# Optimization experiments

Hardware: AMD Instinct MI355X
Metric: run time of the kernel (lower is better)

## Reference

```python
import jax, jax.numpy as jnp
import numpy as np

B, N, D = 4, 2048, 1024
H, HD = 16, 64          # heads, head dim
ROT = 64                # rotary dims (full head)
SCALE = HD ** -0.5


def _rotate_half(x):
    # interleaved pair rotation: (c r) with r=2 -> (-x2, x1)
    x = x.reshape(x.shape[:-1] + (-1, 2))
    x1, x2 = x[..., 0], x[..., 1]
    return jnp.stack((-x2, x1), axis=-1).reshape(x.shape[:-2] + (-1,))


def _rope(t, pos_enc):
    # t: [b,h,n,c], pos_enc: [1,n,rot] -> broadcast over heads
    pe = pos_enc[:, None, : t.shape[-2], :]          # [1,1,n,rot]
    t_rot, t_pass = t[..., :ROT], t[..., ROT:]
    t_rot = t_rot * jnp.cos(pe) + _rotate_half(t_rot) * jnp.sin(pe)
    return jnp.concatenate((t_rot, t_pass), axis=-1)


def setup_inputs() -> dict:
    key = jax.random.key(0)
    ks = jax.random.split(key, 16)
    s = 0.02
    return {
        "query": jax.random.normal(ks[0], (B, N, D), jnp.float32),
        "key": jax.random.normal(ks[1], (B, N, D), jnp.float32),
        "value": jax.random.normal(ks[2], (B, N, D), jnp.float32),
        "pad_mask": jax.random.randint(ks[3], (B, N), 0, 2) > 0,
        "pos_enc": jax.random.uniform(ks[4], (1, N, ROT), jnp.float32),
        "Wq": jax.random.normal(ks[5], (D, D), jnp.float32) * s,
        "bq": jnp.zeros((D,), jnp.float32),
        "Wk": jax.random.normal(ks[6], (D, D), jnp.float32) * s,
        "bk": jnp.zeros((D,), jnp.float32),
        "Wv": jax.random.normal(ks[7], (D, D), jnp.float32) * s,
        "bv": jnp.zeros((D,), jnp.float32),
        "Wo": jax.random.normal(ks[8], (D, D), jnp.float32) * s,
        "bo": jnp.zeros((D,), jnp.float32),
    }


def reference(query, key, value, pad_mask, pos_enc, Wq, bq, Wk, bk, Wv, bv, Wo, bo):
    def split_heads(x):
        return x.reshape(x.shape[0], x.shape[1], H, HD).transpose(0, 2, 1, 3)  # b h n c

    q = split_heads(query @ Wq + bq) * SCALE
    k = split_heads(key @ Wk + bk)
    v = split_heads(value @ Wv + bv)

    q = _rope(q, pos_enc)
    k = _rope(k, pos_enc)

    attn = jnp.einsum("bhic,bhjc->bhij", q, k)
    neg = -jnp.finfo(attn.dtype).max
    attn = jnp.where(pad_mask[:, None, None, :], neg, attn)
    attn = jax.nn.softmax(attn, axis=-1)

    o = jnp.einsum("bhij,bhjc->bhic", attn, v)
    o = o.transpose(0, 2, 1, 3).reshape(o.shape[0], o.shape[2], H * HD)  # b n (h c)
    return o @ Wo + bo
```

## Files before the change

kernel.cpp:

```cpp
#include <hip/hip_runtime.h>

#define B_ 4
#define N_ 2048
#define D_ 1024
#define H_ 16
#define HD_ 64
#define QSCALE_ 0.18033688011112042f

typedef __bf16 bf16x8 __attribute__((ext_vector_type(8)));
typedef float f32x4 __attribute__((ext_vector_type(4)));

#if __has_builtin(__builtin_amdgcn_exp2f)
#define EXP2(x) __builtin_amdgcn_exp2f(x)
#else
#define EXP2(x) exp2f(x)
#endif

__device__ __forceinline__ f32x4 mfma16(bf16x8 a, bf16x8 b, f32x4 c) {
    return __builtin_amdgcn_mfma_f32_16x16x32_bf16(a, b, c, 0, 0, 0);
}

__device__ __forceinline__ void gload16(const void* g, void* l) {
    __builtin_amdgcn_global_load_lds(
        (const __attribute__((address_space(1))) void*)g,
        (__attribute__((address_space(3))) void*)l, 16, 0, 0);
}

__device__ __forceinline__ unsigned pack2(float x, float y) {
    __bf16 a = (__bf16)x, b = (__bf16)y;
    unsigned ua = __builtin_bit_cast(unsigned short, a);
    unsigned ub = __builtin_bit_cast(unsigned short, b);
    return ua | (ub << 16);
}

__global__ __launch_bounds__(256) void pre_kernel(
    const float* __restrict__ q, const float* __restrict__ k, const float* __restrict__ v,
    __bf16* __restrict__ xb,
    const float* __restrict__ W0, const float* __restrict__ W1,
    const float* __restrict__ W2, const float* __restrict__ W3,
    __bf16* __restrict__ T0, __bf16* __restrict__ T1,
    __bf16* __restrict__ T2, __bf16* __restrict__ T3,
    const float* __restrict__ pe, const int* __restrict__ mask,
    unsigned* __restrict__ cstab, float* __restrict__ maskf)
{
    const int y = blockIdx.y;
    const int x = blockIdx.x;
    const int t = threadIdx.x;

    if (y < 3) {
        const float* src = (y == 0) ? q : (y == 1) ? k : v;
        __bf16* dst = xb + (size_t)y * 8388608;
        size_t i = ((size_t)x * 256 + t) * 8;
        float4 a = *(const float4*)(src + i);
        float4 b = *(const float4*)(src + i + 4);
        bf16x8 o;
        o[0] = (__bf16)a.x; o[1] = (__bf16)a.y; o[2] = (__bf16)a.z; o[3] = (__bf16)a.w;
        o[4] = (__bf16)b.x; o[5] = (__bf16)b.y; o[6] = (__bf16)b.z; o[7] = (__bf16)b.w;
        *(bf16x8*)(dst + i) = o;
        return;
    }
    if (x < 1024) {
        const int which = x >> 8;
        const float* W = (which == 0) ? W0 : (which == 1) ? W1 : (which == 2) ? W2 : W3;
        __bf16* Wt = (which == 0) ? T0 : (which == 1) ? T1 : (which == 2) ? T2 : T3;
        const int k0 = ((x >> 4) & 15) * 64, n0 = (x & 15) * 64;
        __shared__ float T[64][65];
#pragma unroll
        for (int i = 0; i < 4; ++i) {
            int row = i * 16 + (t >> 4);
            int c4 = (t & 15) * 4;
            float4 vv = *(const float4*)(W + (size_t)(k0 + row) * D_ + n0 + c4);
            T[row][c4] = vv.x; T[row][c4 + 1] = vv.y; T[row][c4 + 2] = vv.z; T[row][c4 + 3] = vv.w;
        }
        __syncthreads();
#pragma unroll
        for (int i = 0; i < 2; ++i) {
            int task = i * 256 + t;
            int nrow = task >> 3, ks = task & 7;
            bf16x8 o;
#pragma unroll
            for (int e = 0; e < 8; ++e) o[e] = (__bf16)T[ks * 8 + e][nrow];
            *(bf16x8*)(Wt + (size_t)(n0 + nrow) * D_ + k0 + ks * 8) = o;
        }
        return;
    }
    if (x < 1568) {
        int i = (x - 1024) * 256 + t;
        if (i < N_ * HD_) {
            float vv = pe[i];
            __bf16 cb = (__bf16)cosf(vv), sb = (__bf16)sinf(vv);
            unsigned cu = __builtin_bit_cast(unsigned short, cb);
            unsigned su = __builtin_bit_cast(unsigned short, sb);
            cstab[i] = cu | (su << 16);
        }
        if (i < B_ * N_) maskf[i] = mask[i] ? -1e30f : 0.0f;
    }
}

__global__ void prep_kernel(const float* __restrict__ pe, const int* __restrict__ mask,
                            unsigned* __restrict__ cstab, float* __restrict__ maskf) {
    int i = blockIdx.x * 256 + threadIdx.x;
    if (i < N_ * HD_) {
        float v = pe[i];
        __bf16 cb = (__bf16)cosf(v), sb = (__bf16)sinf(v);
        unsigned cu = __builtin_bit_cast(unsigned short, cb);
        unsigned su = __builtin_bit_cast(unsigned short, sb);
        cstab[i] = cu | (su << 16);
    }
    if (i < B_ * N_) maskf[i] = mask[i] ? -1e30f : 0.0f;
}

__global__ __launch_bounds__(256) void tw_kernel(const float* __restrict__ W, __bf16* __restrict__ Wt) {
    __shared__ float T[64][65];
    const int k0 = blockIdx.x * 64, n0 = blockIdx.y * 64;
    const int t = threadIdx.x;
#pragma unroll
    for (int i = 0; i < 4; ++i) {
        int row = i * 16 + (t >> 4);
        int c4 = (t & 15) * 4;
        float4 v = *(const float4*)(W + (size_t)(k0 + row) * D_ + n0 + c4);
        T[row][c4] = v.x; T[row][c4 + 1] = v.y; T[row][c4 + 2] = v.z; T[row][c4 + 3] = v.w;
    }
    __syncthreads();
#pragma unroll
    for (int i = 0; i < 2; ++i) {
        int task = i * 256 + t;
        int nrow = task >> 3, ks = task & 7;
        bf16x8 o;
#pragma unroll
        for (int e = 0; e < 8; ++e) o[e] = (__bf16)T[ks * 8 + e][nrow];
        *(bf16x8*)(Wt + (size_t)(n0 + nrow) * D_ + k0 + ks * 8) = o;
    }
}

__global__ __launch_bounds__(256) void tw3_kernel(
    const float* __restrict__ W0, const float* __restrict__ W1, const float* __restrict__ W2,
    __bf16* __restrict__ T0, __bf16* __restrict__ T1, __bf16* __restrict__ T2)
{
    const float* W = (blockIdx.z == 0) ? W0 : (blockIdx.z == 1) ? W1 : W2;
    __bf16* Wt = (blockIdx.z == 0) ? T0 : (blockIdx.z == 1) ? T1 : T2;
    __shared__ float T[64][65];
    const int k0 = blockIdx.x * 64, n0 = blockIdx.y * 64;
    const int t = threadIdx.x;
#pragma unroll
    for (int i = 0; i < 4; ++i) {
        int row = i * 16 + (t >> 4);
        int c4 = (t & 15) * 4;
        float4 v = *(const float4*)(W + (size_t)(k0 + row) * D_ + n0 + c4);
        T[row][c4] = v.x; T[row][c4 + 1] = v.y; T[row][c4 + 2] = v.z; T[row][c4 + 3] = v.w;
    }
    __syncthreads();
#pragma unroll
    for (int i = 0; i < 2; ++i) {
        int task = i * 256 + t;
        int nrow = task >> 3, ks = task & 7;
        bf16x8 o;
#pragma unroll
        for (int e = 0; e < 8; ++e) o[e] = (__bf16)T[ks * 8 + e][nrow];
        *(bf16x8*)(Wt + (size_t)(n0 + nrow) * D_ + k0 + ks * 8) = o;
    }
}

__global__ __launch_bounds__(256) void proj_v6(
    const __bf16* __restrict__ Xb,
    const __bf16* __restrict__ WtQ, const __bf16* __restrict__ WtK, const __bf16* __restrict__ WtV,
    const float* __restrict__ bQ, const float* __restrict__ bK, const float* __restrict__ bV,
    const unsigned* __restrict__ cstab,
    __bf16* __restrict__ dq, __bf16* __restrict__ dk, __bf16* __restrict__ dv)
{
    __shared__ __align__(16) char smem[35072];
    __bf16* As = (__bf16*)smem;
    __bf16* Bs = (__bf16*)(smem + 16384);

    const int which = blockIdx.y >> 3;
    const __bf16* X   = Xb + (size_t)which * 8388608;
    const __bf16* Wt  = (which == 0) ? WtQ : (which == 1) ? WtK : WtV;
    const float* bias = (which == 0) ? bQ  : (which == 1) ? bK  : bV;
    __bf16* dst       = (which == 0) ? dq  : (which == 1) ? dk  : dv;
    const int mode = which;

    const int tid = threadIdx.x;
    const int lane = tid & 63, w = tid >> 6;
    const int wr = w >> 1, wc = w & 1;
    const int r16 = lane & 15, g = lane >> 4;
    const int m0 = blockIdx.x * 128;
    const int n0 = (blockIdx.y & 7) * 128;
    const int srow8 = tid >> 3, slot = tid & 7;

    f32x4 acc[4][4];
#pragma unroll
    for (int m = 0; m < 4; ++m)
#pragma unroll
        for (int n = 0; n < 4; ++n) acc[m][n] = (f32x4){0.f, 0.f, 0.f, 0.f};

    for (int kt = 0; kt < 16; ++kt) {
#pragma unroll
        for (int j = 0; j < 4; ++j) {
            int row = j * 32 + srow8;
            const char* srcA = (const char*)X + ((size_t)(m0 + row) * D_ + kt * 64) * 2
                               + ((slot ^ (row & 7)) << 4);
            gload16(srcA, (char*)As + j * 4096 + w * 1024);
            const char* srcB = (const char*)Wt + ((size_t)(n0 + row) * D_ + kt * 64) * 2
                               + ((slot ^ (row & 7)) << 4);
            gload16(srcB, (char*)Bs + j * 4096 + w * 1024);
        }
        __syncthreads();
#pragma unroll
        for (int kk = 0; kk < 2; ++kk) {
            bf16x8 aF[4], bF[4];
#pragma unroll
            for (int m = 0; m < 4; ++m) {
                int row = wr * 64 + m * 16 + r16;
                aF[m] = *(const bf16x8*)((char*)As + row * 128 + (((kk * 4 + g) ^ (row & 7)) << 4));
            }
#pragma unroll
            for (int n = 0; n < 4; ++n) {
                int row = wc * 64 + n * 16 + r16;
                bF[n] = *(const bf16x8*)((char*)Bs + row * 128 + (((kk * 4 + g) ^ (row & 7)) << 4));
            }
#pragma unroll
            for (int m = 0; m < 4; ++m)
#pragma unroll
                for (int n = 0; n < 4; ++n)
                    acc[m][n] = mfma16(aF[m], bF[n], acc[m][n]);
        }
        __syncthreads();
    }

    if (mode <= 1) {
#pragma unroll
        for (int m = 0; m < 4; ++m)
#pragma unroll
            for (int n = 0; n < 4; ++n) {
                int col = n0 + wc * 64 + n * 16 + r16;
                int h = col >> 6, hd = col & 63;
#pragma unroll
                for (int j = 0; j < 4; ++j) {
                    int bn = m0 + wr * 64 + m * 16 + g * 4 + j;
                    int np = bn & (N_ - 1), b = bn >> 11;
                    float val = acc[m][n][j] + bias[col];
                    if (mode == 0) val *= QSCALE_;
                    float other = __shfl_xor(val, 1);
                    unsigned cs = cstab[np * HD_ + hd];
                    float c = __uint_as_float(cs << 16);
                    float sn = __uint_as_float(cs & 0xffff0000u);
                    val = val * c + ((col & 1) ? other : -other) * sn;
                    dst[((size_t)(b * H_ + h) * N_ + np) * HD_ + hd] = (__bf16)val;
                }
            }
    } else {
        __bf16* T = (__bf16*)smem;
        __syncthreads();
#pragma unroll
        for (int m = 0; m < 4; ++m)
#pragma unroll
            for (int n = 0; n < 4; ++n) {
                int c = wc * 64 + n * 16 + r16;
                float bs = bias[n0 + c];
#pragma unroll
                for (int j = 0; j < 4; ++j) {
                    int sr = wr * 64 + m * 16 + g * 4 + j;
                    T[c * 136 + sr] = (__bf16)(acc[m][n][j] + bs);
                }
            }
        __syncthreads();
        const int b = m0 >> 11, np0 = m0 & (N_ - 1);
#pragma unroll
        for (int i = 0; i < 8; ++i) {
            int task = i * 256 + tid;
            int trow = task >> 4, ch = task & 15;
            int colg = n0 + trow;
            int h = colg >> 6, hd = colg & 63;
            bf16x8 vv = *(const bf16x8*)&T[trow * 136 + ch * 8];
            *(bf16x8*)(dst + (((size_t)(b * H_ + h) * HD_ + hd) * N_ + np0 + ch * 8)) = vv;
        }
    }
}

__global__ __launch_bounds__(256) void proj_v5(
    const float* __restrict__ Xq, const float* __restrict__ Xk, const float* __restrict__ Xv,
    const __bf16* __restrict__ WtQ, const __bf16* __restrict__ WtK, const __bf16* __restrict__ WtV,
    const float* __restrict__ bQ, const float* __restrict__ bK, const float* __restrict__ bV,
    const unsigned* __restrict__ cstab,
    __bf16* __restrict__ dq, __bf16* __restrict__ dk, __bf16* __restrict__ dv)
{
    __shared__ __align__(16) char smem[35072];
    __bf16* As = (__bf16*)smem;
    __bf16* Bs = (__bf16*)(smem + 16384);

    const int which = blockIdx.y >> 3;
    const float* X    = (which == 0) ? Xq  : (which == 1) ? Xk  : Xv;
    const __bf16* Wt  = (which == 0) ? WtQ : (which == 1) ? WtK : WtV;
    const float* bias = (which == 0) ? bQ  : (which == 1) ? bK  : bV;
    __bf16* dst       = (which == 0) ? dq  : (which == 1) ? dk  : dv;
    const int mode = which;

    const int tid = threadIdx.x;
    const int lane = tid & 63, w = tid >> 6;
    const int wr = w >> 1, wc = w & 1;
    const int r16 = lane & 15, g = lane >> 4;
    const int m0 = blockIdx.x * 128;
    const int n0 = (blockIdx.y & 7) * 128;
    const int srow8 = tid >> 3, slot = tid & 7;

    f32x4 acc[4][4];
#pragma unroll
    for (int m = 0; m < 4; ++m)
#pragma unroll
        for (int n = 0; n < 4; ++n) acc[m][n] = (f32x4){0.f, 0.f, 0.f, 0.f};

    for (int kt = 0; kt < 16; ++kt) {
        float4 va0[4], va1[4];
#pragma unroll
        for (int i = 0; i < 4; ++i) {
            int row = i * 32 + srow8;
            const float* s = X + (size_t)(m0 + row) * D_ + kt * 64 + slot * 8;
            va0[i] = *(const float4*)s;
            va1[i] = *(const float4*)(s + 4);
        }
#pragma unroll
        for (int j = 0; j < 4; ++j) {
            int row = j * 32 + srow8;
            const char* src = (const char*)Wt + ((size_t)(n0 + row) * D_ + kt * 64) * 2
                              + ((slot ^ (row & 7)) << 4);
            gload16(src, (char*)Bs + j * 4096 + w * 1024);
        }
#pragma unroll
        for (int i = 0; i < 4; ++i) {
            int row = i * 32 + srow8;
            bf16x8 bv;
            bv[0] = (__bf16)va0[i].x; bv[1] = (__bf16)va0[i].y;
            bv[2] = (__bf16)va0[i].z; bv[3] = (__bf16)va0[i].w;
            bv[4] = (__bf16)va1[i].x; bv[5] = (__bf16)va1[i].y;
            bv[6] = (__bf16)va1[i].z; bv[7] = (__bf16)va1[i].w;
            *(bf16x8*)((char*)As + row * 128 + ((slot ^ (row & 7)) << 4)) = bv;
        }
        __syncthreads();
#pragma unroll
        for (int kk = 0; kk < 2; ++kk) {
            bf16x8 aF[4], bF[4];
#pragma unroll
            for (int m = 0; m < 4; ++m) {
                int row = wr * 64 + m * 16 + r16;
                aF[m] = *(const bf16x8*)((char*)As + row * 128 + (((kk * 4 + g) ^ (row & 7)) << 4));
            }
#pragma unroll
            for (int n = 0; n < 4; ++n) {
                int row = wc * 64 + n * 16 + r16;
                bF[n] = *(const bf16x8*)((char*)Bs + row * 128 + (((kk * 4 + g) ^ (row & 7)) << 4));
            }
#pragma unroll
            for (int m = 0; m < 4; ++m)
#pragma unroll
                for (int n = 0; n < 4; ++n)
                    acc[m][n] = mfma16(aF[m], bF[n], acc[m][n]);
        }
        __syncthreads();
    }

    if (mode <= 1) {
#pragma unroll
        for (int m = 0; m < 4; ++m)
#pragma unroll
            for (int n = 0; n < 4; ++n) {
                int col = n0 + wc * 64 + n * 16 + r16;
                int h = col >> 6, hd = col & 63;
#pragma unroll
                for (int j = 0; j < 4; ++j) {
                    int bn = m0 + wr * 64 + m * 16 + g * 4 + j;
                    int np = bn & (N_ - 1), b = bn >> 11;
                    float val = acc[m][n][j] + bias[col];
                    if (mode == 0) val *= QSCALE_;
                    float other = __shfl_xor(val, 1);
                    unsigned cs = cstab[np * HD_ + hd];
                    float c = __uint_as_float(cs << 16);
                    float sn = __uint_as_float(cs & 0xffff0000u);
                    val = val * c + ((col & 1) ? other : -other) * sn;
                    dst[((size_t)(b * H_ + h) * N_ + np) * HD_ + hd] = (__bf16)val;
                }
            }
    } else {
        __bf16* T = (__bf16*)smem;
        __syncthreads();
#pragma unroll
        for (int m = 0; m < 4; ++m)
#pragma unroll
            for (int n = 0; n < 4; ++n) {
                int c = wc * 64 + n * 16 + r16;
                float bs = bias[n0 + c];
#pragma unroll
                for (int j = 0; j < 4; ++j) {
                    int sr = wr * 64 + m * 16 + g * 4 + j;
                    T[c * 136 + sr] = (__bf16)(acc[m][n][j] + bs);
                }
            }
        __syncthreads();
        const int b = m0 >> 11, np0 = m0 & (N_ - 1);
#pragma unroll
        for (int i = 0; i < 8; ++i) {
            int task = i * 256 + tid;
            int trow = task >> 4, ch = task & 15;
            int colg = n0 + trow;
            int h = colg >> 6, hd = colg & 63;
            bf16x8 vv = *(const bf16x8*)&T[trow * 136 + ch * 8];
            *(bf16x8*)(dst + (((size_t)(b * H_ + h) * HD_ + hd) * N_ + np0 + ch * 8)) = vv;
        }
    }
}

__global__ __launch_bounds__(512, 4) void attn_v8(
    const __bf16* __restrict__ qws, const __bf16* __restrict__ kws,
    const __bf16* __restrict__ vtws, const float* __restrict__ maskf,
    __bf16* __restrict__ ows)
{
    __shared__ __align__(16) __bf16 Ks0[4096], Ks1[4096];
    __shared__ __align__(16) __bf16 Vs0[4096], Vs1[4096];
    __shared__ __align__(16) char Pbuf[16384];

    const int tid = threadIdx.x;
    const int lane = tid & 63, w = tid >> 6;
    const int r16 = lane & 15, g = lane >> 4;

    const int lid = blockIdx.x;
    const int virt = (lid & 7) * 64 + (lid >> 3);
    const int bh = virt >> 3;
    const int b = bh >> 4, h = bh & 15;
    const int q0 = (virt & 7) * 256;
    const int srow8 = tid >> 3, slot = tid & 7;

    bf16x8 qF[2][2];
#pragma unroll
    for (int qq = 0; qq < 2; ++qq) {
        const __bf16* qb = qws + ((size_t)bh * N_ + q0 + w * 32 + qq * 16 + r16) * HD_ + g * 8;
        qF[qq][0] = *(const bf16x8*)qb;
        qF[qq][1] = *(const bf16x8*)(qb + 32);
    }

    bf16x8 onesF;
#pragma unroll
    for (int e = 0; e < 8; ++e) onesF[e] = (__bf16)1.0f;

    const char* kbase = (const char*)(kws + (size_t)bh * N_ * HD_);
    const char* vbase = (const char*)(vtws + (size_t)bh * HD_ * N_);
    const float* mbase = maskf + b * N_;
    char* Pw = Pbuf + w * 2048;

    f32x4 o[2][4];
    f32x4 lacc[2];
#pragma unroll
    for (int qq = 0; qq < 2; ++qq) {
        lacc[qq] = (f32x4){0.f, 0.f, 0.f, 0.f};
#pragma unroll
        for (int n = 0; n < 4; ++n) o[qq][n] = (f32x4){0.f, 0.f, 0.f, 0.f};
    }

#define STAGE_(KD, VD, kt) {                                                          \
    gload16(kbase + (size_t)((kt) * 64 + srow8) * 128 + ((slot ^ (srow8 & 7)) << 4),  \
            (char*)(KD) + w * 1024);                                                  \
    gload16(vbase + (size_t)srow8 * (N_ * 2) + (kt) * 128 + ((slot ^ (srow8 & 7)) << 4), \
            (char*)(VD) + w * 1024);                                                  \
    }

#define TILE_(KB, VB, KN, VN, kt) {                                                   \
    if ((kt) + 1 < 32) STAGE_(KN, VN, (kt) + 1);                                      \
    f32x4 s0[4], s1[4];                                                               \
    _Pragma("unroll")                                                                 \
    for (int n = 0; n < 4; ++n) {                                                     \
        f32x4 mb = *(const f32x4*)(mbase + (kt) * 64 + n * 16 + g * 4);               \
        s0[n] = mb; s1[n] = mb;                                                       \
    }                                                                                 \
    __builtin_amdgcn_s_setprio(1);                                                    \
    _Pragma("unroll")                                                                 \
    for (int n = 0; n < 4; ++n) {                                                     \
        int row = n * 16 + r16;                                                       \
        bf16x8 kF0 = *(const bf16x8*)((const char*)(KB) + row * 128 + ((g ^ (row & 7)) << 4));        \
        bf16x8 kF1 = *(const bf16x8*)((const char*)(KB) + row * 128 + (((4 + g) ^ (row & 7)) << 4));  \
        s0[n] = mfma16(kF0, qF[0][0], s0[n]);                                         \
        s0[n] = mfma16(kF1, qF[0][1], s0[n]);                                         \
        s1[n] = mfma16(kF0, qF[1][0], s1[n]);                                         \
        s1[n] = mfma16(kF1, qF[1][1], s1[n]);                                         \
    }                                                                                 \
    __builtin_amdgcn_s_setprio(0);                                                    \
    bf16x8 pF0[2], pF1[2];                                                            \
    _Pragma("unroll")                                                                 \
    for (int n = 0; n < 4; ++n) {                                                     \
        int u0 = ((n * 2 + (g >> 1)) ^ (r16 & 7));                                    \
        int off = (g & 1) * 2;                                                        \
        *(unsigned*)(Pw + r16 * 128 + u0 * 16 + off * 4)       = pack2(EXP2(s0[n][0]), EXP2(s0[n][1])); \
        *(unsigned*)(Pw + r16 * 128 + u0 * 16 + (off + 1) * 4) = pack2(EXP2(s0[n][2]), EXP2(s0[n][3])); \
    }                                                                                 \
    _Pragma("unroll")                                                                 \
    for (int kk = 0; kk < 2; ++kk)                                                    \
        pF0[kk] = *(const bf16x8*)(Pw + r16 * 128 + (((kk * 4 + g) ^ (r16 & 7)) << 4)); \
    lacc[0] = mfma16(onesF, pF0[0], lacc[0]);                                         \
    lacc[0] = mfma16(onesF, pF0[1], lacc[0]);                                         \
    _Pragma("unroll")                                                                 \
    for (int n = 0; n < 4; ++n) {                                                     \
        int u0 = ((n * 2 + (g >> 1)) ^ (r16 & 7));                                    \
        int off = (g & 1) * 2;                                                        \
        *(unsigned*)(Pw + r16 * 128 + u0 * 16 + off * 4)       = pack2(EXP2(s1[n][0]), EXP2(s1[n][1])); \
        *(unsigned*)(Pw + r16 * 128 + u0 * 16 + (off + 1) * 4) = pack2(EXP2(s1[n][2]), EXP2(s1[n][3])); \
    }                                                                                 \
    _Pragma("unroll")                                                                 \
    for (int kk = 0; kk < 2; ++kk)                                                    \
        pF1[kk] = *(const bf16x8*)(Pw + r16 * 128 + (((kk * 4 + g) ^ (r16 & 7)) << 4)); \
    lacc[1] = mfma16(onesF, pF1[0], lacc[1]);                                         \
    lacc[1] = mfma16(onesF, pF1[1], lacc[1]);                                         \
    __builtin_amdgcn_s_setprio(1);                                                    \
    _Pragma("unroll")                                                                 \
    for (int n = 0; n < 4; ++n) {                                                     \
        int row = n * 16 + r16;                                                       \
        bf16x8 vF0 = *(const bf16x8*)((const char*)(VB) + row * 128 + ((g ^ (row & 7)) << 4));        \
        bf16x8 vF1 = *(const bf16x8*)((const char*)(VB) + row * 128 + (((4 + g) ^ (row & 7)) << 4));  \
        o[0][n] = mfma16(vF0, pF0[0], o[0][n]);                                       \
        o[0][n] = mfma16(vF1, pF0[1], o[0][n]);                                       \
        o[1][n] = mfma16(vF0, pF1[0], o[1][n]);                                       \
        o[1][n] = mfma16(vF1, pF1[1], o[1][n]);                                       \
    }                                                                                 \
    __builtin_amdgcn_s_setprio(0);                                                    \
    __syncthreads(); }

    STAGE_(Ks0, Vs0, 0);
    __syncthreads();

    for (int kt = 0; kt < 32; kt += 2) {
        TILE_(Ks0, Vs0, Ks1, Vs1, kt);
        TILE_(Ks1, Vs1, Ks0, Vs0, kt + 1);
    }
#undef TILE_
#undef STAGE_

#pragma unroll
    for (int qq = 0; qq < 2; ++qq) {
        float inv = 1.0f / lacc[qq][0];
#pragma unroll
        for (int n = 0; n < 4; ++n) {
            int u0 = ((n * 2 + (g >> 1)) ^ (r16 & 7));
            int off = (g & 1) * 2;
            *(unsigned*)(Pw + r16 * 128 + u0 * 16 + off * 4)       = pack2(o[qq][n][0] * inv, o[qq][n][1] * inv);
            *(unsigned*)(Pw + r16 * 128 + u0 * 16 + (off + 1) * 4) = pack2(o[qq][n][2] * inv, o[qq][n][3] * inv);
        }
        int qrow = q0 + w * 32 + qq * 16 + r16;
#pragma unroll
        for (int kk = 0; kk < 2; ++kk) {
            bf16x8 v = *(const bf16x8*)(Pw + r16 * 128 + (((kk * 4 + g) ^ (r16 & 7)) << 4));
            *(bf16x8*)(ows + ((size_t)(b * N_ + qrow)) * D_ + h * HD_ + kk * 32 + g * 8) = v;
        }
    }
}

__global__ __launch_bounds__(256) void gemm_out_v2(
    const __bf16* __restrict__ A, const __bf16* __restrict__ Wt,
    const float* __restrict__ bias, float* __restrict__ out)
{
    __shared__ __align__(16) __bf16 As[8192], Bs[8192];

    const int tid = threadIdx.x;
    const int lane = tid & 63, w = tid >> 6;
    const int wr = w >> 1, wc = w & 1;
    const int r16 = lane & 15, g = lane >> 4;
    const int m0 = blockIdx.x * 128;
    const int n0 = blockIdx.y * 128;
    const int srow8 = tid >> 3, slot = tid & 7;

    f32x4 acc[4][4];
#pragma unroll
    for (int m = 0; m < 4; ++m)
#pragma unroll
        for (int n = 0; n < 4; ++n) acc[m][n] = (f32x4){0.f, 0.f, 0.f, 0.f};

    for (int kt = 0; kt < 16; ++kt) {
#pragma unroll
        for (int j = 0; j < 4; ++j) {
            int row = j * 32 + srow8;
            const char* srcA = (const char*)A + ((size_t)(m0 + row) * D_ + kt * 64) * 2
                               + ((slot ^ (row & 7)) << 4);
            gload16(srcA, (char*)As + j * 4096 + w * 1024);
            const char* srcB = (const char*)Wt + ((size_t)(n0 + row) * D_ + kt * 64) * 2
                               + ((slot ^ (row & 7)) << 4);
            gload16(srcB, (char*)Bs + j * 4096 + w * 1024);
        }
        __syncthreads();
#pragma unroll
        for (int kk = 0; kk < 2; ++kk) {
            bf16x8 aF[4], bF[4];
#pragma unroll
            for (int m = 0; m < 4; ++m) {
                int row = wr * 64 + m * 16 + r16;
                aF[m] = *(const bf16x8*)((char*)As + row * 128 + (((kk * 4 + g) ^ (row & 7)) << 4));
            }
#pragma unroll
            for (int n = 0; n < 4; ++n) {
                int row = wc * 64 + n * 16 + r16;
                bF[n] = *(const bf16x8*)((char*)Bs + row * 128 + (((kk * 4 + g) ^ (row & 7)) << 4));
            }
#pragma unroll
            for (int m = 0; m < 4; ++m)
#pragma unroll
                for (int n = 0; n < 4; ++n)
                    acc[m][n] = mfma16(aF[m], bF[n], acc[m][n]);
        }
        __syncthreads();
    }

#pragma unroll
    for (int m = 0; m < 4; ++m)
#pragma unroll
        for (int n = 0; n < 4; ++n) {
            int col = n0 + wc * 64 + n * 16 + r16;
            float bs = bias[col];
#pragma unroll
            for (int j = 0; j < 4; ++j) {
                int bn = m0 + wr * 64 + m * 16 + g * 4 + j;
                out[(size_t)bn * D_ + col] = acc[m][n][j] + bs;
            }
        }
}

extern "C" void kernel_launch(void* const* d_in, const int* in_sizes, int n_in,
                              void* d_out, int out_size, void* d_ws, size_t ws_size,
                              hipStream_t stream)
{
    const float* query = (const float*)d_in[0];
    const float* key   = (const float*)d_in[1];
    const float* value = (const float*)d_in[2];
    const int* mask    = (const int*)d_in[3];
    const float* pos_enc = (const float*)d_in[4];
    const float* Wq = (const float*)d_in[5];
    const float* bq = (const float*)d_in[6];
    const float* Wk = (const float*)d_in[7];
    const float* bk = (const float*)d_in[8];
    const float* Wv = (const float*)d_in[9];
    const float* bv = (const float*)d_in[10];
    const float* Wo = (const float*)d_in[11];
    const float* bo = (const float*)d_in[12];
    float* out = (float*)d_out;

    char* ws = (char*)d_ws;
    const size_t MB16 = (size_t)16 * 1024 * 1024;
    const size_t MB2  = (size_t)2 * 1024 * 1024;
    const size_t need_big = 3 * MB16 + 4 * MB16 + 4 * MB2 + 524288 + 32768;
    const size_t need_small = 4 * MB16 + 524288 + 32768;

    if (ws_size >= need_big) {
        __bf16* Xb    = (__bf16*)(ws);
        __bf16* qws   = (__bf16*)(ws + 3 * MB16);
        __bf16* kws   = (__bf16*)(ws + 4 * MB16);
        __bf16* vtws  = (__bf16*)(ws + 5 * MB16);
        __bf16* ows   = (__bf16*)(ws + 6 * MB16);
        __bf16* wtQ   = (__bf16*)(ws + 7 * MB16);
        __bf16* wtK   = (__bf16*)(ws + 7 * MB16 + MB2);
        __bf16* wtV   = (__bf16*)(ws + 7 * MB16 + 2 * MB2);
        __bf16* wtO   = (__bf16*)(ws + 7 * MB16 + 3 * MB2);
        unsigned* cstab = (unsigned*)(ws + 7 * MB16 + 4 * MB2);
        float* maskf  = (float*)(ws + 7 * MB16 + 4 * MB2 + 524288);

        hipLaunchKernelGGL(pre_kernel, dim3(4096, 4), dim3(256), 0, stream,
                           query, key, value, Xb, Wq, Wk, Wv, Wo, wtQ, wtK, wtV, wtO,
                           pos_enc, mask, cstab, maskf);
        hipLaunchKernelGGL(proj_v6, dim3(64, 24), dim3(256), 0, stream,
                           Xb, wtQ, wtK, wtV, bq, bk, bv, cstab, qws, kws, vtws);
        hipLaunchKernelGGL(attn_v8, dim3(512), dim3(512), 0, stream,
                           qws, kws, vtws, maskf, ows);
        hipLaunchKernelGGL(gemm_out_v2, dim3(64, 8), dim3(256), 0, stream, ows, wtO, bo, out);
    } else {
        if (ws_size < need_small) return;
        __bf16* qws   = (__bf16*)(ws);
        __bf16* kws   = (__bf16*)(ws + MB16);
        __bf16* vtws  = (__bf16*)(ws + 2 * MB16);
        __bf16* ows   = (__bf16*)(ws + 3 * MB16);
        unsigned* cstab = (unsigned*)(ws + 4 * MB16);
        float* maskf  = (float*)(ws + 4 * MB16 + 524288);
        __bf16* wtQ   = (__bf16*)(ws + 3 * MB16);
        __bf16* wtK   = wtQ + (size_t)D_ * D_;
        __bf16* wtV   = wtK + (size_t)D_ * D_;
        __bf16* wtO   = (__bf16*)(ws);

        hipLaunchKernelGGL(prep_kernel, dim3(512), dim3(256), 0, stream, pos_enc, mask, cstab, maskf);
        hipLaunchKernelGGL(tw3_kernel, dim3(16, 16, 3), dim3(256), 0, stream, Wq, Wk, Wv, wtQ, wtK, wtV);
        hipLaunchKernelGGL(proj_v5, dim3(64, 24), dim3(256), 0, stream,
                           query, key, value, wtQ, wtK, wtV, bq, bk, bv, cstab, qws, kws, vtws);
        hipLaunchKernelGGL(attn_v8, dim3(512), dim3(512), 0, stream,
                           qws, kws, vtws, maskf, ows);
        hipLaunchKernelGGL(tw_kernel, dim3(16, 16), dim3(256), 0, stream, Wo, wtO);
        hipLaunchKernelGGL(gemm_out_v2, dim3(64, 8), dim3(256), 0, stream, ows, wtO, bo, out);
    }
}
```

Measured before the change: 206.4 us.

## Halve attention query tile per block and double grid size

Measured after the change: 227.2 us. 1.1x slower.

```diff
diff --git a/kernel.cpp b/kernel.cpp
--- a/kernel.cpp
+++ b/kernel.cpp
@@ -408,7 +408,7 @@
     }
 }
 
-__global__ __launch_bounds__(512, 4) void attn_v8(
+__global__ __launch_bounds__(512, 4) void attn_v9(
     const __bf16* __restrict__ qws, const __bf16* __restrict__ kws,
     const __bf16* __restrict__ vtws, const float* __restrict__ maskf,
     __bf16* __restrict__ ows)
@@ -422,18 +422,17 @@
     const int r16 = lane & 15, g = lane >> 4;
 
     const int lid = blockIdx.x;
-    const int virt = (lid & 7) * 64 + (lid >> 3);
-    const int bh = virt >> 3;
+    const int virt = (lid & 7) * 128 + (lid >> 3);
+    const int bh = virt >> 4;
     const int b = bh >> 4, h = bh & 15;
-    const int q0 = (virt & 7) * 256;
+    const int q0 = (virt & 15) * 128;
     const int srow8 = tid >> 3, slot = tid & 7;
 
-    bf16x8 qF[2][2];
-#pragma unroll
-    for (int qq = 0; qq < 2; ++qq) {
-        const __bf16* qb = qws + ((size_t)bh * N_ + q0 + w * 32 + qq * 16 + r16) * HD_ + g * 8;
-        qF[qq][0] = *(const bf16x8*)qb;
-        qF[qq][1] = *(const bf16x8*)(qb + 32);
+    bf16x8 qF0, qF1;
+    {
+        const __bf16* qb = qws + ((size_t)bh * N_ + q0 + w * 16 + r16) * HD_ + g * 8;
+        qF0 = *(const bf16x8*)qb;
+        qF1 = *(const bf16x8*)(qb + 32);
     }
 
     bf16x8 onesF;
@@ -445,14 +444,10 @@
     const float* mbase = maskf + b * N_;
     char* Pw = Pbuf + w * 2048;
 
-    f32x4 o[2][4];
-    f32x4 lacc[2];
-#pragma unroll
-    for (int qq = 0; qq < 2; ++qq) {
-        lacc[qq] = (f32x4){0.f, 0.f, 0.f, 0.f};
-#pragma unroll
-        for (int n = 0; n < 4; ++n) o[qq][n] = (f32x4){0.f, 0.f, 0.f, 0.f};
-    }
+    f32x4 o[4];
+    f32x4 lacc = (f32x4){0.f, 0.f, 0.f, 0.f};
+#pragma unroll
+    for (int n = 0; n < 4; ++n) o[n] = (f32x4){0.f, 0.f, 0.f, 0.f};
 
 #define STAGE_(KD, VD, kt) {                                                          \
     gload16(kbase + (size_t)((kt) * 64 + srow8) * 128 + ((slot ^ (srow8 & 7)) << 4),  \
@@ -463,59 +458,42 @@
 
 #define TILE_(KB, VB, KN, VN, kt) {                                                   \
     if ((kt) + 1 < 32) STAGE_(KN, VN, (kt) + 1);                                      \
-    f32x4 s0[4], s1[4];                                                               \
+    f32x4 s[4];                                                                       \
     _Pragma("unroll")                                                                 \
-    for (int n = 0; n < 4; ++n) {                                                     \
-        f32x4 mb = *(const f32x4*)(mbase + (kt) * 64 + n * 16 + g * 4);               \
-        s0[n] = mb; s1[n] = mb;                                                       \
-    }                                                                                 \
+    for (int n = 0; n < 4; ++n)                                                       \
+        s[n] = *(const f32x4*)(mbase + (kt) * 64 + n * 16 + g * 4);                   \
     __builtin_amdgcn_s_setprio(1);                                                    \
     _Pragma("unroll")                                                                 \
     for (int n = 0; n < 4; ++n) {                                                     \
         int row = n * 16 + r16;                                                       \
         bf16x8 kF0 = *(const bf16x8*)((const char*)(KB) + row * 128 + ((g ^ (row & 7)) << 4));        \
         bf16x8 kF1 = *(const bf16x8*)((const char*)(KB) + row * 128 + (((4 + g) ^ (row & 7)) << 4));  \
-        s0[n] = mfma16(kF0, qF[0][0], s0[n]);                                         \
-        s0[n] = mfma16(kF1, qF[0][1], s0[n]);                                         \
-        s1[n] = mfma16(kF0, qF[1][0], s1[n]);                                         \
-        s1[n] = mfma16(kF1, qF[1][1], s1[n]);                                         \
+        s[n] = mfma16(kF0, qF0, s[n]);                                                \
+        s[n] = mfma16(kF1, qF1, s[n]);                                                \
     }                                                                                 \
     __builtin_amdgcn_s_setprio(0);                                                    \
-    bf16x8 pF0[2], pF1[2];                                                            \
+    bf16x8 pF[2];                                                                     \
     _Pragma("unroll")                                                                 \
     for (int n = 0; n < 4; ++n) {                                                     \
         int u0 = ((n * 2 + (g >> 1)) ^ (r16 & 7));                                    \
-        int off = (g & 1) * 2;                                                        \
-        *(unsigned*)(Pw + r16 * 128 + u0 * 16 + off * 4)       = pack2(EXP2(s0[n][0]), EXP2(s0[n][1])); \
-        *(unsigned*)(Pw + r16 * 128 + u0 * 16 + (off + 1) * 4) = pack2(EXP2(s0[n][2]), EXP2(s0[n][3])); \
+        unsigned lo = pack2(EXP2(s[n][0]), EXP2(s[n][1]));                            \
+        unsigned hi = pack2(EXP2(s[n][2]), EXP2(s[n][3]));                            \
+        *(unsigned long long*)(Pw + r16 * 128 + u0 * 16 + (g & 1) * 8) =              \
+            ((unsigned long long)hi << 32) | lo;                                      \
     }                                                                                 \
     _Pragma("unroll")                                                                 \
     for (int kk = 0; kk < 2; ++kk)                                                    \
-        pF0[kk] = *(const bf16x8*)(Pw + r16 * 128 + (((kk * 4 + g) ^ (r16 & 7)) << 4)); \
-    lacc[0] = mfma16(onesF, pF0[0], lacc[0]);                                         \
-    lacc[0] = mfma16(onesF, pF0[1], lacc[0]);                                         \
-    _Pragma("unroll")                                                                 \
-    for (int n = 0; n < 4; ++n) {                                                     \
-        int u0 = ((n * 2 + (g >> 1)) ^ (r16 & 7));                                    \
-        int off = (g & 1) * 2;                                                        \
-        *(unsigned*)(Pw + r16 * 128 + u0 * 16 + off * 4)       = pack2(EXP2(s1[n][0]), EXP2(s1[n][1])); \
-        *(unsigned*)(Pw + r16 * 128 + u0 * 16 + (off + 1) * 4) = pack2(EXP2(s1[n][2]), EXP2(s1[n][3])); \
-    }                                                                                 \
-    _Pragma("unroll")                                                                 \
-    for (int kk = 0; kk < 2; ++kk)                                                    \
-        pF1[kk] = *(const bf16x8*)(Pw + r16 * 128 + (((kk * 4 + g) ^ (r16 & 7)) << 4)); \
-    lacc[1] = mfma16(onesF, pF1[0], lacc[1]);                                         \
-    lacc[1] = mfma16(onesF, pF1[1], lacc[1]);                                         \
+        pF[kk] = *(const bf16x8*)(Pw + r16 * 128 + (((kk * 4 + g) ^ (r16 & 7)) << 4)); \
+    lacc = mfma16(onesF, pF[0], lacc);                                                \
+    lacc = mfma16(onesF, pF[1], lacc);                                                \
     __builtin_amdgcn_s_setprio(1);                                                    \
     _Pragma("unroll")                                                                 \
     for (int n = 0; n < 4; ++n) {                                                     \
         int row = n * 16 + r16;                                                       \
         bf16x8 vF0 = *(const bf16x8*)((const char*)(VB) + row * 128 + ((g ^ (row & 7)) << 4));        \
         bf16x8 vF1 = *(const bf16x8*)((const char*)(VB) + row * 128 + (((4 + g) ^ (row & 7)) << 4));  \
-        o[0][n] = mfma16(vF0, pF0[0], o[0][n]);                                       \
-        o[0][n] = mfma16(vF1, pF0[1], o[0][n]);                                       \
-        o[1][n] = mfma16(vF0, pF1[0], o[1][n]);                                       \
-        o[1][n] = mfma16(vF1, pF1[1], o[1][n]);                                       \
+        o[n] = mfma16(vF0, pF[0], o[n]);                                              \
+        o[n] = mfma16(vF1, pF[1], o[n]);                                              \
     }                                                                                 \
     __builtin_amdgcn_s_setprio(0);                                                    \
     __syncthreads(); }
@@ -530,17 +508,17 @@
 #undef TILE_
 #undef STAGE_
 
-#pragma unroll
-    for (int qq = 0; qq < 2; ++qq) {
-        float inv = 1.0f / lacc[qq][0];
+    {
+        float inv = 1.0f / lacc[0];
 #pragma unroll
         for (int n = 0; n < 4; ++n) {
             int u0 = ((n * 2 + (g >> 1)) ^ (r16 & 7));
-            int off = (g & 1) * 2;
-            *(unsigned*)(Pw + r16 * 128 + u0 * 16 + off * 4)       = pack2(o[qq][n][0] * inv, o[qq][n][1] * inv);
-            *(unsigned*)(Pw + r16 * 128 + u0 * 16 + (off + 1) * 4) = pack2(o[qq][n][2] * inv, o[qq][n][3] * inv);
-        }
-        int qrow = q0 + w * 32 + qq * 16 + r16;
+            unsigned lo = pack2(o[n][0] * inv, o[n][1] * inv);
+            unsigned hi = pack2(o[n][2] * inv, o[n][3] * inv);
+            *(unsigned long long*)(Pw + r16 * 128 + u0 * 16 + (g & 1) * 8) =
+                ((unsigned long long)hi << 32) | lo;
+        }
+        int qrow = q0 + w * 16 + r16;
 #pragma unroll
         for (int kk = 0; kk < 2; ++kk) {
             bf16x8 v = *(const bf16x8*)(Pw + r16 * 128 + (((kk * 4 + g) ^ (r16 & 7)) << 4));
@@ -660,7 +638,7 @@
                            pos_enc, mask, cstab, maskf);
         hipLaunchKernelGGL(proj_v6, dim3(64, 24), dim3(256), 0, stream,
                            Xb, wtQ, wtK, wtV, bq, bk, bv, cstab, qws, kws, vtws);
-        hipLaunchKernelGGL(attn_v8, dim3(512), dim3(512), 0, stream,
+        hipLaunchKernelGGL(attn_v9, dim3(1024), dim3(512), 0, stream,
                            qws, kws, vtws, maskf, ows);
         hipLaunchKernelGGL(gemm_out_v2, dim3(64, 8), dim3(256), 0, stream, ows, wtO, bo, out);
     } else {
@@ -680,7 +658,7 @@
         hipLaunchKernelGGL(tw3_kernel, dim3(16, 16, 3), dim3(256), 0, stream, Wq, Wk, Wv, wtQ, wtK, wtV);
         hipLaunchKernelGGL(proj_v5, dim3(64, 24), dim3(256), 0, stream,
                            query, key, value, wtQ, wtK, wtV, bq, bk, bv, cstab, qws, kws, vtws);
-        hipLaunchKernelGGL(attn_v8, dim3(512), dim3(512), 0, stream,
+        hipLaunchKernelGGL(attn_v9, dim3(1024), dim3(512), 0, stream,
                            qws, kws, vtws, maskf, ows);
         hipLaunchKernelGGL(tw_kernel, dim3(16, 16), dim3(256), 0, stream, Wo, wtO);
         hipLaunchKernelGGL(gemm_out_v2, dim3(64, 8), dim3(256), 0, stream, ows, wtO, bo, out);
```
